# Kernel optimization log

Measured on AMD Instinct MI355X. Metric: run time of the kernel, lower is better.

Reference implementation:

```python
import jax, jax.numpy as jnp
import numpy as np

B, S, D, H = 64, 512, 256, 512

def setup_inputs() -> dict:
    key = jax.random.key(0)
    ks = jax.random.split(key, 16)
    s_in = 1.0 / np.sqrt(D)
    s_h = 1.0 / np.sqrt(H)
    inp = {
        "inputs": jax.random.normal(ks[0], (B, S, D), jnp.float32),
        # input-side gate weights (stored [D,H], equiv to torch Linear weight.T)
        "Wf": jax.random.uniform(ks[1], (D, H), jnp.float32, -s_in, s_in),
        "Wi": jax.random.uniform(ks[2], (D, H), jnp.float32, -s_in, s_in),
        "Wo": jax.random.uniform(ks[3], (D, H), jnp.float32, -s_in, s_in),
        "Wc": jax.random.uniform(ks[4], (D, H), jnp.float32, -s_in, s_in),
        "bf": jax.random.uniform(ks[5], (H,), jnp.float32, -s_in, s_in),
        "bi": jax.random.uniform(ks[6], (H,), jnp.float32, -s_in, s_in),
        "bo": jax.random.uniform(ks[7], (H,), jnp.float32, -s_in, s_in),
        "bc": jax.random.uniform(ks[8], (H,), jnp.float32, -s_in, s_in),
        # recurrent weights (bias=False)
        "Uf": jax.random.uniform(ks[9], (H, H), jnp.float32, -s_h, s_h),
        "Ui": jax.random.uniform(ks[10], (H, H), jnp.float32, -s_h, s_h),
        "Uo": jax.random.uniform(ks[11], (H, H), jnp.float32, -s_h, s_h),
        "Uc": jax.random.uniform(ks[12], (H, H), jnp.float32, -s_h, s_h),
        # output head
        "Wfc": jax.random.uniform(ks[13], (H, 1), jnp.float32, -s_h, s_h),
        "bfc": jax.random.uniform(ks[14], (1,), jnp.float32, -s_h, s_h),
    }
    return inp


def reference(inputs, Wf, Wi, Wo, Wc, bf, bi, bo, bc, Uf, Ui, Uo, Uc, Wfc, bfc):
    # Precompute all input-side gate projections in one big GEMM: [B,S,4H]
    Wx = jnp.concatenate([Wf, Wi, Wo, Wc], axis=1)            # [D,4H]
    bx = jnp.concatenate([bf, bi, bo, bc], axis=0)            # [4H]
    gx = jnp.einsum('bsd,dg->bsg', inputs, Wx) + bx           # [B,S,4H]
    Uh = jnp.concatenate([Uf, Ui, Uo, Uc], axis=1)            # [H,4H]

    h0 = jnp.zeros((inputs.shape[0], Uf.shape[0]), inputs.dtype)
    c0 = jnp.zeros_like(h0)
    Hd = Uf.shape[0]

    def step(carry, gx_t):
        h, c = carry
        g = gx_t + h @ Uh                                     # [B,4H]
        f_t = jax.nn.sigmoid(g[:, 0 * Hd:1 * Hd])
        i_t = jax.nn.sigmoid(g[:, 1 * Hd:2 * Hd])
        o_t = jax.nn.sigmoid(g[:, 2 * Hd:3 * Hd])
        chat = jnp.tanh(g[:, 3 * Hd:4 * Hd])
        c = f_t * c + i_t * chat
        h = o_t * jnp.tanh(c)
        return (h, c), h

    (h_t, c_t), hs = jax.lax.scan(step, (h0, c0), jnp.swapaxes(gx, 0, 1))
    outputs = jnp.swapaxes(hs, 0, 1)                          # [B,S,H]
    predictions = jnp.einsum('bsh,ho->bso', outputs, Wfc) + bfc
    return predictions, h_t, c_t
```

## Files before the change

### kernel.cpp

```cpp
#include <hip/hip_runtime.h>
#include <hip/hip_bf16.h>

#define B_ 64
#define S_ 512
#define D_ 256
#define H_ 512

typedef __attribute__((ext_vector_type(8))) short bf16x8;
typedef __attribute__((ext_vector_type(4))) float f32x4;
typedef __attribute__((ext_vector_type(4))) unsigned int uint4v;
typedef unsigned short ushort_t;

__device__ __forceinline__ ushort_t f2bf(float f) {
    __hip_bfloat16 h = __float2bfloat16(f);
    return *reinterpret_cast<ushort_t*>(&h);
}
__device__ __forceinline__ float sigmoid_f(float x) { return 1.f / (1.f + __expf(-x)); }
__device__ __forceinline__ float tanh_f(float x) { return 1.f - 2.f / (__expf(2.f * x) + 1.f); }

__global__ __launch_bounds__(512, 2) void lstm_rec(
    const float* __restrict__ X,
    const float* __restrict__ Wf, const float* __restrict__ Wi,
    const float* __restrict__ Wo, const float* __restrict__ Wc,
    const float* __restrict__ bfp, const float* __restrict__ bip,
    const float* __restrict__ bop, const float* __restrict__ bcp,
    const float* __restrict__ Uf, const float* __restrict__ Ui,
    const float* __restrict__ Uo, const float* __restrict__ Uc,
    const float* __restrict__ Wfc,
    float* __restrict__ pred, unsigned int* __restrict__ hbufU,
    unsigned int* __restrict__ cnt,
    float* __restrict__ outH, float* __restrict__ outC)
{
    __shared__ ushort_t hS[16 * 520];
    __shared__ ushort_t xS[16 * 264];
    __shared__ float gact[4][16][68];

    const int tid  = threadIdx.x;
    const int w    = tid >> 6;
    const int lane = tid & 63;
    const int q    = lane >> 4;
    const int m    = lane & 15;
    const int gate = w >> 1;
    const int half = w & 1;
    const int g    = blockIdx.x & 3;
    const int s    = blockIdx.x >> 2;

    const int ncol0 = s * 64 + half * 32 + m;
    const int ncol1 = ncol0 + 16;

    const float* Ug = (gate == 0) ? Uf : (gate == 1) ? Ui : (gate == 2) ? Uo : Uc;
    const float* Wg = (gate == 0) ? Wf : (gate == 1) ? Wi : (gate == 2) ? Wo : Wc;
    const float* bg = (gate == 0) ? bfp : (gate == 1) ? bip : (gate == 2) ? bop : bcp;

    const float bias0 = bg[ncol0];
    const float bias1 = bg[ncol1];

    bf16x8 UF[2][16];
    bf16x8 WF[2][8];
    #pragma unroll
    for (int tt = 0; tt < 2; ++tt) {
        const int nc = tt ? ncol1 : ncol0;
        #pragma unroll
        for (int ks = 0; ks < 16; ++ks) {
            bf16x8 v;
            #pragma unroll
            for (int j = 0; j < 8; ++j) {
                int k = ks * 32 + q * 8 + j;
                v[j] = (short)f2bf(Ug[k * H_ + nc]);
            }
            UF[tt][ks] = v;
        }
        #pragma unroll
        for (int ks = 0; ks < 8; ++ks) {
            bf16x8 v;
            #pragma unroll
            for (int j = 0; j < 8; ++j) {
                int k = ks * 32 + q * 8 + j;
                v[j] = (short)f2bf(Wg[k * H_ + nc]);
            }
            WF[tt][ks] = v;
        }
    }

    const int urow  = tid >> 5;
    const int upair = tid & 31;
    const float2 wfc2 = *(const float2*)&Wfc[s * 64 + 2 * upair];

    float cr0 = 0.f, cr1 = 0.f;
    float pv_prev = 0.f;

    {
        const float* xsrc = &X[((size_t)(g * 16 + urow) * S_ + 0) * D_ + upair * 8];
        float4 a = *(const float4*)xsrc;
        float4 b = *(const float4*)(xsrc + 4);
        bf16x8 v;
        v[0] = (short)f2bf(a.x); v[1] = (short)f2bf(a.y);
        v[2] = (short)f2bf(a.z); v[3] = (short)f2bf(a.w);
        v[4] = (short)f2bf(b.x); v[5] = (short)f2bf(b.y);
        v[6] = (short)f2bf(b.z); v[7] = (short)f2bf(b.w);
        *(bf16x8*)&xS[urow * 264 + upair * 8] = v;
    }

    float4 xr0, xr1;

    for (int t = 0; t < S_; ++t) {
        if (t > 0 && tid == 0) {
            unsigned int target = 8u * (unsigned int)t;
            while (__hip_atomic_load(&cnt[g * 64], __ATOMIC_RELAXED, __HIP_MEMORY_SCOPE_AGENT) < target) {
                __builtin_amdgcn_s_sleep(1);
            }
        }
        __syncthreads();

        if (t + 1 < S_) {
            const float* xsrc = &X[((size_t)(g * 16 + urow) * S_ + (t + 1)) * D_ + upair * 8];
            xr0 = *(const float4*)xsrc;
            xr1 = *(const float4*)(xsrc + 4);
        }
        {
            const int row  = tid >> 5;
            const int dcol = (tid & 31) * 8;
            const unsigned int* p0 = &hbufU[(size_t)((t % 3) * B_ + g * 16 + row) * 256 + dcol];
            const unsigned int* p1 = p0 + 4;
            uint4v ra, rb;
            asm volatile(
                "global_load_dwordx4 %0, %2, off sc0 sc1\n\t"
                "global_load_dwordx4 %1, %3, off sc0 sc1\n\t"
                "s_waitcnt vmcnt(0)"
                : "=v"(ra), "=v"(rb) : "v"(p0), "v"(p1) : "memory");
            *(uint4v*)&hS[row * 520 + dcol * 2]     = ra;
            *(uint4v*)&hS[row * 520 + dcol * 2 + 8] = rb;
        }
        __syncthreads();

        if (t > 0 && upair == 0) {
            atomicAdd(&pred[(g * 16 + urow) * S_ + (t - 1)], pv_prev);
        }
        f32x4 accA0 = {bias0, bias0, bias0, bias0};
        f32x4 accA1 = {bias1, bias1, bias1, bias1};
        f32x4 accB0 = {0.f, 0.f, 0.f, 0.f};
        f32x4 accB1 = {0.f, 0.f, 0.f, 0.f};
        #pragma unroll
        for (int ks = 0; ks < 8; ++ks) {
            bf16x8 a = *(const bf16x8*)&xS[m * 264 + ks * 32 + q * 8];
            accA0 = __builtin_amdgcn_mfma_f32_16x16x32_bf16(a, WF[0][ks], accA0, 0, 0, 0);
            accA1 = __builtin_amdgcn_mfma_f32_16x16x32_bf16(a, WF[1][ks], accA1, 0, 0, 0);
        }
        #pragma unroll
        for (int ks = 0; ks < 16; ++ks) {
            bf16x8 a = *(const bf16x8*)&hS[m * 520 + ks * 32 + q * 8];
            accB0 = __builtin_amdgcn_mfma_f32_16x16x32_bf16(a, UF[0][ks], accB0, 0, 0, 0);
            accB1 = __builtin_amdgcn_mfma_f32_16x16x32_bf16(a, UF[1][ks], accB1, 0, 0, 0);
        }
        #pragma unroll
        for (int j = 0; j < 4; ++j) {
            float v0 = accA0[j] + accB0[j];
            float v1 = accA1[j] + accB1[j];
            v0 = (gate < 3) ? sigmoid_f(v0) : tanh_f(v0);
            v1 = (gate < 3) ? sigmoid_f(v1) : tanh_f(v1);
            gact[gate][q * 4 + j][half * 32 + m]      = v0;
            gact[gate][q * 4 + j][half * 32 + 16 + m] = v1;
        }
        __syncthreads();

        float2 f2v = *(const float2*)&gact[0][urow][2 * upair];
        float2 i2v = *(const float2*)&gact[1][urow][2 * upair];
        float2 o2v = *(const float2*)&gact[2][urow][2 * upair];
        float2 ch2 = *(const float2*)&gact[3][urow][2 * upair];
        cr0 = f2v.x * cr0 + i2v.x * ch2.x;
        cr1 = f2v.y * cr1 + i2v.y * ch2.y;
        float hv0 = o2v.x * tanh_f(cr0);
        float hv1 = o2v.y * tanh_f(cr1);

        float pv = hv0 * wfc2.x + hv1 * wfc2.y;
        pv += __shfl_xor(pv, 16);
        pv += __shfl_xor(pv, 8);
        pv += __shfl_xor(pv, 4);
        pv += __shfl_xor(pv, 2);
        pv += __shfl_xor(pv, 1);
        pv_prev = pv;

        if (t < S_ - 1) {
            unsigned int packed = (unsigned int)f2bf(hv0) | ((unsigned int)f2bf(hv1) << 16);
            __hip_atomic_store(
                &hbufU[(size_t)(((t + 1) % 3) * B_ + g * 16 + urow) * 256 + s * 32 + upair],
                packed, __ATOMIC_RELAXED, __HIP_MEMORY_SCOPE_AGENT);

            bf16x8 v;
            v[0] = (short)f2bf(xr0.x); v[1] = (short)f2bf(xr0.y);
            v[2] = (short)f2bf(xr0.z); v[3] = (short)f2bf(xr0.w);
            v[4] = (short)f2bf(xr1.x); v[5] = (short)f2bf(xr1.y);
            v[6] = (short)f2bf(xr1.z); v[7] = (short)f2bf(xr1.w);
            *(bf16x8*)&xS[urow * 264 + upair * 8] = v;

            __syncthreads();
            if (tid == 0) {
                __hip_atomic_fetch_add(&cnt[g * 64], 1u, __ATOMIC_RELEASE, __HIP_MEMORY_SCOPE_AGENT);
            }
        } else {
            *(float2*)&outH[(g * 16 + urow) * H_ + s * 64 + 2 * upair] = make_float2(hv0, hv1);
            *(float2*)&outC[(g * 16 + urow) * H_ + s * 64 + 2 * upair] = make_float2(cr0, cr1);
            if (upair == 0) atomicAdd(&pred[(g * 16 + urow) * S_ + t], pv_prev);
        }
    }
}

__global__ void pred_fin(const float* __restrict__ pred,
                         const float* __restrict__ bfc,
                         float* __restrict__ out)
{
    int i = blockIdx.x * blockDim.x + threadIdx.x;
    if (i < B_ * S_) out[i] = pred[i] + bfc[0];
}

extern "C" void kernel_launch(void* const* d_in, const int* in_sizes, int n_in,
                              void* d_out, int out_size, void* d_ws, size_t ws_size,
                              hipStream_t stream) {
    const float* X   = (const float*)d_in[0];
    const float* Wf  = (const float*)d_in[1];
    const float* Wi  = (const float*)d_in[2];
    const float* Wo  = (const float*)d_in[3];
    const float* Wc  = (const float*)d_in[4];
    const float* bfp = (const float*)d_in[5];
    const float* bip = (const float*)d_in[6];
    const float* bop = (const float*)d_in[7];
    const float* bcp = (const float*)d_in[8];
    const float* Uf  = (const float*)d_in[9];
    const float* Ui  = (const float*)d_in[10];
    const float* Uo  = (const float*)d_in[11];
    const float* Uc  = (const float*)d_in[12];
    const float* Wfc = (const float*)d_in[13];
    const float* bfc = (const float*)d_in[14];

    float*        pred  = (float*)d_ws;
    unsigned int* hbufU = (unsigned int*)((char*)d_ws + 131072);
    unsigned int* cnt   = (unsigned int*)((char*)d_ws + 131072 + 196608);

    hipMemsetAsync(d_ws, 0, 131072 + 196608 + 1024, stream);

    float* out = (float*)d_out;
    lstm_rec<<<32, 512, 0, stream>>>(X, Wf, Wi, Wo, Wc, bfp, bip, bop, bcp,
                                     Uf, Ui, Uo, Uc, Wfc,
                                     pred, hbufU, cnt,
                                     out + 32768, out + 65536);
    pred_fin<<<128, 256, 0, stream>>>(pred, bfc, out);
}
```

Before: 2.411 ms.

## Replace block counter barrier with per-wave flags and lighter LDS barriers

Result: no change. 2.425 ms (+0.6%).

```diff
diff --git a/kernel.cpp b/kernel.cpp
--- a/kernel.cpp
+++ b/kernel.cpp
@@ -17,6 +17,10 @@
 }
 __device__ __forceinline__ float sigmoid_f(float x) { return 1.f / (1.f + __expf(-x)); }
 __device__ __forceinline__ float tanh_f(float x) { return 1.f - 2.f / (__expf(2.f * x) + 1.f); }
+
+__device__ __forceinline__ void lds_barrier() {
+    asm volatile("s_waitcnt lgkmcnt(0)\n\ts_barrier" ::: "memory");
+}
 
 __global__ __launch_bounds__(512, 2) void lstm_rec(
     const float* __restrict__ X,
@@ -28,7 +32,7 @@
     const float* __restrict__ Uo, const float* __restrict__ Uc,
     const float* __restrict__ Wfc,
     float* __restrict__ pred, unsigned int* __restrict__ hbufU,
-    unsigned int* __restrict__ cnt,
+    unsigned int* __restrict__ flags,
     float* __restrict__ outH, float* __restrict__ outC)
 {
     __shared__ ushort_t hS[16 * 520];
@@ -64,20 +68,16 @@
         for (int ks = 0; ks < 16; ++ks) {
             bf16x8 v;
             #pragma unroll
-            for (int j = 0; j < 8; ++j) {
-                int k = ks * 32 + q * 8 + j;
-                v[j] = (short)f2bf(Ug[k * H_ + nc]);
-            }
+            for (int j = 0; j < 8; ++j)
+                v[j] = (short)f2bf(Ug[(ks * 32 + q * 8 + j) * H_ + nc]);
             UF[tt][ks] = v;
         }
         #pragma unroll
         for (int ks = 0; ks < 8; ++ks) {
             bf16x8 v;
             #pragma unroll
-            for (int j = 0; j < 8; ++j) {
-                int k = ks * 32 + q * 8 + j;
-                v[j] = (short)f2bf(Wg[k * H_ + nc]);
-            }
+            for (int j = 0; j < 8; ++j)
+                v[j] = (short)f2bf(Wg[(ks * 32 + q * 8 + j) * H_ + nc]);
             WF[tt][ks] = v;
         }
     }
@@ -87,7 +87,9 @@
     const float2 wfc2 = *(const float2*)&Wfc[s * 64 + 2 * upair];
 
     float cr0 = 0.f, cr1 = 0.f;
-    float pv_prev = 0.f;
+
+    unsigned int* flagsG = flags + g * 64;
+    const int myflag = s * 8 + w;
 
     {
         const float* xsrc = &X[((size_t)(g * 16 + urow) * S_ + 0) * D_ + upair * 8];
@@ -104,19 +106,16 @@
     float4 xr0, xr1;
 
     for (int t = 0; t < S_; ++t) {
-        if (t > 0 && tid == 0) {
-            unsigned int target = 8u * (unsigned int)t;
-            while (__hip_atomic_load(&cnt[g * 64], __ATOMIC_RELAXED, __HIP_MEMORY_SCOPE_AGENT) < target) {
+        if (t > 0) {
+            const unsigned int tgt = (unsigned int)t;
+            for (;;) {
+                unsigned int f = __hip_atomic_load(&flagsG[lane],
+                                                   __ATOMIC_RELAXED, __HIP_MEMORY_SCOPE_AGENT);
+                if (__ballot(f >= tgt) == ~0ull) break;
                 __builtin_amdgcn_s_sleep(1);
             }
         }
-        __syncthreads();
-
-        if (t + 1 < S_) {
-            const float* xsrc = &X[((size_t)(g * 16 + urow) * S_ + (t + 1)) * D_ + upair * 8];
-            xr0 = *(const float4*)xsrc;
-            xr1 = *(const float4*)(xsrc + 4);
-        }
+
         {
             const int row  = tid >> 5;
             const int dcol = (tid & 31) * 8;
@@ -131,10 +130,12 @@
             *(uint4v*)&hS[row * 520 + dcol * 2]     = ra;
             *(uint4v*)&hS[row * 520 + dcol * 2 + 8] = rb;
         }
-        __syncthreads();
-
-        if (t > 0 && upair == 0) {
-            atomicAdd(&pred[(g * 16 + urow) * S_ + (t - 1)], pv_prev);
+        lds_barrier();
+
+        if (t + 1 < S_) {
+            const float* xsrc = &X[((size_t)(g * 16 + urow) * S_ + (t + 1)) * D_ + upair * 8];
+            xr0 = *(const float4*)xsrc;
+            xr1 = *(const float4*)(xsrc + 4);
         }
         f32x4 accA0 = {bias0, bias0, bias0, bias0};
         f32x4 accA1 = {bias1, bias1, bias1, bias1};
@@ -161,7 +162,7 @@
             gact[gate][q * 4 + j][half * 32 + m]      = v0;
             gact[gate][q * 4 + j][half * 32 + 16 + m] = v1;
         }
-        __syncthreads();
+        lds_barrier();
 
         float2 f2v = *(const float2*)&gact[0][urow][2 * upair];
         float2 i2v = *(const float2*)&gact[1][urow][2 * upair];
@@ -173,35 +174,34 @@
         float hv1 = o2v.y * tanh_f(cr1);
 
         float pv = hv0 * wfc2.x + hv1 * wfc2.y;
-        pv += __shfl_xor(pv, 16);
-        pv += __shfl_xor(pv, 8);
-        pv += __shfl_xor(pv, 4);
-        pv += __shfl_xor(pv, 2);
-        pv += __shfl_xor(pv, 1);
-        pv_prev = pv;
 
         if (t < S_ - 1) {
             unsigned int packed = (unsigned int)f2bf(hv0) | ((unsigned int)f2bf(hv1) << 16);
             __hip_atomic_store(
                 &hbufU[(size_t)(((t + 1) % 3) * B_ + g * 16 + urow) * 256 + s * 32 + upair],
                 packed, __ATOMIC_RELAXED, __HIP_MEMORY_SCOPE_AGENT);
-
+            asm volatile("s_waitcnt vmcnt(0)" ::: "memory");
+            if (lane == 0) {
+                __hip_atomic_store(&flagsG[myflag], (unsigned int)(t + 1),
+                                   __ATOMIC_RELAXED, __HIP_MEMORY_SCOPE_AGENT);
+            }
             bf16x8 v;
             v[0] = (short)f2bf(xr0.x); v[1] = (short)f2bf(xr0.y);
             v[2] = (short)f2bf(xr0.z); v[3] = (short)f2bf(xr0.w);
             v[4] = (short)f2bf(xr1.x); v[5] = (short)f2bf(xr1.y);
             v[6] = (short)f2bf(xr1.z); v[7] = (short)f2bf(xr1.w);
             *(bf16x8*)&xS[urow * 264 + upair * 8] = v;
-
-            __syncthreads();
-            if (tid == 0) {
-                __hip_atomic_fetch_add(&cnt[g * 64], 1u, __ATOMIC_RELEASE, __HIP_MEMORY_SCOPE_AGENT);
-            }
         } else {
             *(float2*)&outH[(g * 16 + urow) * H_ + s * 64 + 2 * upair] = make_float2(hv0, hv1);
             *(float2*)&outC[(g * 16 + urow) * H_ + s * 64 + 2 * upair] = make_float2(cr0, cr1);
-            if (upair == 0) atomicAdd(&pred[(g * 16 + urow) * S_ + t], pv_prev);
-        }
+        }
+
+        pv += __shfl_xor(pv, 16);
+        pv += __shfl_xor(pv, 8);
+        pv += __shfl_xor(pv, 4);
+        pv += __shfl_xor(pv, 2);
+        pv += __shfl_xor(pv, 1);
+        if (upair == 0) atomicAdd(&pred[(g * 16 + urow) * S_ + t], pv);
     }
 }
 
@@ -234,14 +234,14 @@
 
     float*        pred  = (float*)d_ws;
     unsigned int* hbufU = (unsigned int*)((char*)d_ws + 131072);
-    unsigned int* cnt   = (unsigned int*)((char*)d_ws + 131072 + 196608);
-
-    hipMemsetAsync(d_ws, 0, 131072 + 196608 + 1024, stream);
+    unsigned int* flags = (unsigned int*)((char*)d_ws + 131072 + 196608);
+
+    hipMemsetAsync(d_ws, 0, 131072 + 196608 + 2048, stream);
 
     float* out = (float*)d_out;
     lstm_rec<<<32, 512, 0, stream>>>(X, Wf, Wi, Wo, Wc, bfp, bip, bop, bcp,
                                      Uf, Ui, Uo, Uc, Wfc,
-                                     pred, hbufU, cnt,
+                                     pred, hbufU, flags,
                                      out + 32768, out + 65536);
     pred_fin<<<128, 256, 0, stream>>>(pred, bfc, out);
 }
```
